# Kernel optimization log

Hardware: AMD Instinct MI355X
Metric: run time of the kernel (lower is better)

## Reference

```python
import jax, jax.numpy as jnp
import numpy as np

B, T, E, A, D, S, N, K = 256, 64, 1024, 32, 1024, 256, 1024, 5
MIN_STD = 0.1


def setup_inputs() -> dict:
    key = jax.random.key(0)
    ks = jax.random.split(key, 16)
    def w(k, shape, scale=0.02):
        return jax.random.normal(k, shape, jnp.float32) * scale
    return dict(
        seq_len=T,
        obs_embed=jax.random.normal(ks[0], (B, T, E), jnp.float32),
        action=jax.random.normal(ks[1], (B, T, A), jnp.float32),
        nonterms=jnp.ones((B, T, 1), jnp.float32),
        init_deter=jax.random.normal(ks[2], (B, D), jnp.float32),
        init_stoch=jax.random.normal(ks[3], (B, S), jnp.float32),
        noise_prior=jax.random.normal(ks[4], (T - 1, B, S), jnp.float32),
        noise_post=jax.random.normal(ks[5], (T - 1, B, S), jnp.float32),
        W_embed=w(ks[6], (S + A, D)), b_embed=jnp.zeros((D,), jnp.float32),
        W_ens=w(ks[7], (K, D, S)), b_ens=jnp.zeros((K, S), jnp.float32),
        W_ih=w(ks[8], (3 * D, D)), W_hh=w(ks[9], (3 * D, D)),
        b_ih=jnp.zeros((3 * D,), jnp.float32), b_hh=jnp.zeros((3 * D,), jnp.float32),
        Wp1=w(ks[10], (D, N)), bp1=jnp.zeros((N,), jnp.float32),
        Wp2=w(ks[11], (N, 2 * S)), bp2=jnp.zeros((2 * S,), jnp.float32),
        Wq1=w(ks[12], (D + E, N)), bq1=jnp.zeros((N,), jnp.float32),
        Wq2=w(ks[13], (N, 2 * S)), bq2=jnp.zeros((2 * S,), jnp.float32),
    )


def _rollout(obs_embed, action, nonterms, init_deter, init_stoch,
             noise_prior, noise_post, W_embed, b_embed, W_ens, b_ens,
             W_ih, W_hh, b_ih, b_hh, Wp1, bp1, Wp2, bp2, Wq1, bq1, Wq2, bq2):
    elu = jax.nn.elu

    def gru(x, h):  # torch.nn.GRUCell math
        gi = x @ W_ih.T + b_ih
        gh = h @ W_hh.T + b_hh
        ir, iz, ig = jnp.split(gi, 3, axis=-1)
        hr, hz, hg = jnp.split(gh, 3, axis=-1)
        r = jax.nn.sigmoid(ir + hr)
        z = jax.nn.sigmoid(iz + hz)
        n = jnp.tanh(ig + r * hg)
        return (1.0 - z) * n + z * h

    def step(carry, xs):
        deter, stoch = carry
        obs_t, act_t, nt, eps_p, eps_q = xs  # nt: [B,1]
        prev_action = act_t * nt
        sa = elu(jnp.concatenate([stoch * nt, prev_action], -1) @ W_embed + b_embed)
        preds = jnp.einsum('bd,kds->kbs', sa, W_ens) + b_ens[:, None, :]  # ensemble heads
        deter_new = gru(sa, deter * nt)
        pm, ps = jnp.split(elu(deter_new @ Wp1 + bp1) @ Wp2 + bp2, 2, -1)
        ps = jax.nn.softplus(ps) + MIN_STD
        prior_stoch = pm + ps * eps_p
        qm, qs = jnp.split(elu(jnp.concatenate([deter_new, obs_t], -1) @ Wq1 + bq1) @ Wq2 + bq2, 2, -1)
        qs = jax.nn.softplus(qs) + MIN_STD
        post_stoch = qm + qs * eps_q
        prior_cat = jnp.concatenate([pm, ps, prior_stoch, deter_new], -1)   # [B, 3S+D]
        post_cat = jnp.concatenate([qm, qs, post_stoch, deter_new], -1)     # [B, 3S+D]
        disag_flat = jnp.transpose(preds, (1, 0, 2)).reshape(preds.shape[1], -1)  # [B, K*S]
        out = jnp.concatenate([prior_cat, post_cat, disag_flat], -1)
        return (deter_new, post_stoch), out

    Tm1 = noise_prior.shape[0]
    xs = (jnp.swapaxes(obs_embed[:, :Tm1], 0, 1),
          jnp.swapaxes(action[:, :Tm1], 0, 1),
          jnp.swapaxes(nonterms[:, :Tm1], 0, 1),
          noise_prior, noise_post)
    _, outs = jax.lax.scan(step, (init_deter, init_stoch), xs)
    return jnp.swapaxes(outs, 0, 1)  # [B, T-1, 2*(3S+D)+K*S]


def reference(seq_len, obs_embed, action, nonterms, init_deter, init_stoch,
              noise_prior, noise_post, W_embed, b_embed, W_ens, b_ens,
              W_ih, W_hh, b_ih, b_hh, Wp1, bp1, Wp2, bp2, Wq1, bq1, Wq2, bq2):
    return _rollout(obs_embed, action, nonterms, init_deter, init_stoch,
                    noise_prior, noise_post, W_embed, b_embed, W_ens, b_ens,
                    W_ih, W_hh, b_ih, b_hh, Wp1, bp1, Wp2, bp2, Wq1, bq1, Wq2, bq2)
```

## Files before the change

kernel.cpp:

```cpp
#include <hip/hip_runtime.h>

typedef float f32x4 __attribute__((ext_vector_type(4)));
typedef __bf16 bf16x8 __attribute__((ext_vector_type(8)));
typedef unsigned short u16;

#define OUTC 4864
#define OUTT ((size_t)63 * OUTC)

__device__ __forceinline__ u16 f2bf(float f) {
    unsigned u = __float_as_uint(f);
    u += 0x7FFFu + ((u >> 16) & 1u);
    return (u16)(u >> 16);
}
__device__ __forceinline__ float bf2f(u16 h) { return __uint_as_float((unsigned)h << 16); }
__device__ __forceinline__ float fexp(float x) { return __expf(x); }
__device__ __forceinline__ float eluf(float x) { return x > 0.f ? x : fexp(x) - 1.f; }
__device__ __forceinline__ float splus(float x) { return x > 15.f ? x : __logf(1.f + fexp(x)); }
__device__ __forceinline__ float sigm(float x) { return 1.f / (1.f + fexp(-x)); }
__device__ __forceinline__ float tanhfast(float x) { return 2.f / (1.f + fexp(-2.f * x)) - 1.f; }
__device__ __forceinline__ int swz(int row, int cb) { return row * 128 + (cb ^ ((row & 7) << 4)); }

template <int NT, class FA, class FE>
__device__ __forceinline__ void gemmN(char* As, FA fa, const u16* __restrict__ Bt,
                                      int ldb, int n0, int nstr, int K, int m0, FE fe) {
    char* Bs = As + 8192;
    const int tid = threadIdx.x;
    const int lane = tid & 63;
    const int w = tid >> 6;
    const int wr = (w >> 1) * 32, wc = (w & 1) * 32;
    f32x4 acc[NT][4];
    f32x4 zf = {0.f, 0.f, 0.f, 0.f};
#pragma unroll
    for (int j = 0; j < NT; j++)
#pragma unroll
        for (int q = 0; q < 4; q++) acc[j][q] = zf;
    const int r0 = tid >> 3;
    const int ke = (tid & 7) * 8;
    const int cb = (tid & 7) * 16;
    uint4 av0 = fa(m0 + r0, ke);
    uint4 av1 = fa(m0 + r0 + 32, ke);
    uint4 bv[NT][2];
#pragma unroll
    for (int j = 0; j < NT; j++) {
        bv[j][0] = *(const uint4*)(Bt + (size_t)(n0 + j * nstr + r0) * ldb + ke);
        bv[j][1] = *(const uint4*)(Bt + (size_t)(n0 + j * nstr + r0 + 32) * ldb + ke);
    }
    for (int k0 = 0; k0 < K; k0 += 64) {
        __syncthreads();
        *(uint4*)(As + swz(r0, cb)) = av0;
        *(uint4*)(As + swz(r0 + 32, cb)) = av1;
#pragma unroll
        for (int j = 0; j < NT; j++) {
            char* B = Bs + j * 8192;
            *(uint4*)(B + swz(r0, cb)) = bv[j][0];
            *(uint4*)(B + swz(r0 + 32, cb)) = bv[j][1];
        }
        __syncthreads();
        if (k0 + 64 < K) {
            int k1 = k0 + 64 + ke;
            av0 = fa(m0 + r0, k1);
            av1 = fa(m0 + r0 + 32, k1);
#pragma unroll
            for (int j = 0; j < NT; j++) {
                bv[j][0] = *(const uint4*)(Bt + (size_t)(n0 + j * nstr + r0) * ldb + k1);
                bv[j][1] = *(const uint4*)(Bt + (size_t)(n0 + j * nstr + r0 + 32) * ldb + k1);
            }
        }
#pragma unroll
        for (int kk = 0; kk < 64; kk += 32) {
            const int fcb = kk * 2 + (lane >> 4) * 16;
            bf16x8 a0 = *(const bf16x8*)(As + swz(wr + (lane & 15), fcb));
            bf16x8 a1 = *(const bf16x8*)(As + swz(wr + 16 + (lane & 15), fcb));
#pragma unroll
            for (int j = 0; j < NT; j++) {
                char* B = Bs + j * 8192;
                bf16x8 b0 = *(const bf16x8*)(B + swz(wc + (lane & 15), fcb));
                bf16x8 b1 = *(const bf16x8*)(B + swz(wc + 16 + (lane & 15), fcb));
                acc[j][0] = __builtin_amdgcn_mfma_f32_16x16x32_bf16(a0, b0, acc[j][0], 0, 0, 0);
                acc[j][1] = __builtin_amdgcn_mfma_f32_16x16x32_bf16(a0, b1, acc[j][1], 0, 0, 0);
                acc[j][2] = __builtin_amdgcn_mfma_f32_16x16x32_bf16(a1, b0, acc[j][2], 0, 0, 0);
                acc[j][3] = __builtin_amdgcn_mfma_f32_16x16x32_bf16(a1, b1, acc[j][3], 0, 0, 0);
            }
        }
    }
    const int er = (lane >> 4) * 4, ec = lane & 15;
#pragma unroll
    for (int q = 0; q < 4; q++) {
        int rr = m0 + wr + (q >> 1) * 16 + er;
        int cc = n0 + wc + (q & 1) * 16 + ec;
#pragma unroll
        for (int r = 0; r < 4; r++) {
            float vals[NT];
#pragma unroll
            for (int j = 0; j < NT; j++) vals[j] = acc[j][q][r];
            fe(rr + r, cc, vals);
        }
    }
}

__global__ void __launch_bounds__(256) k_cast(const float* __restrict__ in,
                                              u16* __restrict__ out, int n) {
    int i = blockIdx.x * 256 + threadIdx.x;
    if (i < n) out[i] = f2bf(in[i]);
}

__global__ void __launch_bounds__(256) k_transpose(const float* __restrict__ in,
                                                   u16* __restrict__ out,
                                                   int R, int C, int Rpad, int total) {
    int i = blockIdx.x * 256 + threadIdx.x;
    if (i >= total) return;
    int r = i % Rpad;
    int bc = i / Rpad;
    int c = bc % C;
    int bb = bc / C;
    out[i] = (r < R) ? f2bf(in[((size_t)bb * R + r) * C + c]) : (u16)0;
}

__global__ void __launch_bounds__(256) k_init(const float* __restrict__ init_deter,
                                              const float* __restrict__ init_stoch,
                                              const float* __restrict__ action,
                                              const float* __restrict__ nonterms,
                                              float* __restrict__ deter,
                                              u16* __restrict__ h_nt,
                                              u16* __restrict__ x_embed) {
    int idx = blockIdx.x * 256 + threadIdx.x;
    int b = idx >> 10, d = idx & 1023;
    float nt0 = nonterms[b * 64];
    float dv = init_deter[idx];
    deter[idx] = dv;
    h_nt[idx] = f2bf(dv * nt0);
    if (d < 256) {
        x_embed[b * 320 + d] = f2bf(init_stoch[b * 256 + d] * nt0);
    } else if (d < 320) {
        int c = d - 256;
        x_embed[b * 320 + d] = (c < 32) ? f2bf(action[(size_t)b * 2048 + c] * nt0) : (u16)0;
    }
}

__global__ void __launch_bounds__(256) k_obsc(const float* __restrict__ obs,
                                              const u16* __restrict__ Wq1o_t,
                                              u16* __restrict__ OBSC) {
    __shared__ char sm[40960];
    int jid = blockIdx.x;
    int rb = jid >> 2, cg = jid & 3;
    int m0 = rb * 64, n0 = cg * 256;
    auto fa = [&](int r, int k) {
        int tt = r >> 8, bb = r & 255;
        const float* p = obs + ((size_t)bb * 64 + tt) * 1024 + k;
        float4 f0 = *(const float4*)p, f1 = *(const float4*)(p + 4);
        union { u16 h[8]; uint4 q; } x;
        x.h[0] = f2bf(f0.x); x.h[1] = f2bf(f0.y); x.h[2] = f2bf(f0.z); x.h[3] = f2bf(f0.w);
        x.h[4] = f2bf(f1.x); x.h[5] = f2bf(f1.y); x.h[6] = f2bf(f1.z); x.h[7] = f2bf(f1.w);
        return x.q;
    };
    auto fe = [&](int r, int n, const float* v) {
#pragma unroll
        for (int j = 0; j < 4; j++) OBSC[(size_t)r * 1024 + n + j * 64] = f2bf(v[j]);
    };
    gemmN<4>(sm, fa, Wq1o_t, 1024, n0, 64, 1024, m0, fe);
}

__global__ void __launch_bounds__(256) k_sa(const u16* __restrict__ xe,
                                            const u16* __restrict__ Wt,
                                            const float* __restrict__ bias,
                                            u16* __restrict__ sa) {
    __shared__ char sm[16384];
    int m0 = blockIdx.y * 64, n0 = blockIdx.x * 64;
    auto fa = [&](int r, int k) { return *(const uint4*)(xe + r * 320 + k); };
    auto fe = [&](int r, int n, const float* v) {
        sa[r * 1024 + n] = f2bf(eluf(v[0] + bias[n]));
    };
    gemmN<1>(sm, fa, Wt, 320, n0, 0, 320, m0, fe);
}

__global__ void __launch_bounds__(256) k_gemm3072(const u16* __restrict__ A,
                                                  const u16* __restrict__ B,
                                                  const float* __restrict__ bias,
                                                  float* __restrict__ dst) {
    __shared__ char sm[16384];
    int m0 = blockIdx.y * 64, n0 = blockIdx.x * 64;
    auto fa = [&](int r, int k) { return *(const uint4*)(A + r * 1024 + k); };
    auto fe = [&](int r, int n, const float* v) { dst[(size_t)r * 3072 + n] = v[0] + bias[n]; };
    gemmN<1>(sm, fa, B, 1024, n0, 0, 1024, m0, fe);
}

__global__ void __launch_bounds__(256) k_gru(const float* __restrict__ gi,
                                             const float* __restrict__ gh,
                                             float* __restrict__ deter,
                                             const float* __restrict__ nonterms, int t,
                                             u16* __restrict__ deter_hist,
                                             u16* __restrict__ h_nt,
                                             float* __restrict__ out) {
    int idx = blockIdx.x * 256 + threadIdx.x;
    int b = idx >> 10, d = idx & 1023;
    float nt = nonterms[b * 64 + t];
    float h = deter[idx] * nt;
    size_t gb = (size_t)b * 3072;
    float r = sigm(gi[gb + d] + gh[gb + d]);
    float z = sigm(gi[gb + 1024 + d] + gh[gb + 1024 + d]);
    float n = tanhfast(gi[gb + 2048 + d] + r * gh[gb + 2048 + d]);
    float dn = (1.f - z) * n + z * h;
    deter[idx] = dn;
    u16 db = f2bf(dn);
    deter_hist[(size_t)t * 262144 + idx] = db;
    h_nt[idx] = f2bf(dn * nonterms[b * 64 + t + 1]);
    float* ob = out + (size_t)b * OUTT + (size_t)t * OUTC;
    ob[768 + d] = dn;
    ob[2560 + d] = dn;
}

__global__ void __launch_bounds__(256) k_step4(const u16* __restrict__ h_nt,
                                               const u16* __restrict__ Whh_b,
                                               const float* __restrict__ b_hh,
                                               float* __restrict__ gh,
                                               const u16* __restrict__ deter_hist,
                                               const u16* __restrict__ Wq1d_t,
                                               const float* __restrict__ bq1,
                                               const u16* __restrict__ OBSC,
                                               u16* __restrict__ HQ, int t) {
    __shared__ char sm[16384];
    int bid = blockIdx.x;
    if (bid < 192) {
        if (t >= 62) return;
        int m0 = (bid / 48) * 64, n0 = (bid % 48) * 64;
        auto fa = [&](int r, int k) { return *(const uint4*)(h_nt + r * 1024 + k); };
        auto fe = [&](int r, int n, const float* v) { gh[(size_t)r * 3072 + n] = v[0] + b_hh[n]; };
        gemmN<1>(sm, fa, Whh_b, 1024, n0, 0, 1024, m0, fe);
    } else {
        int j = bid - 192;
        int m0 = (j / 16) * 64, n0 = (j % 16) * 64;
        const u16* A = deter_hist + (size_t)t * 262144;
        const u16* ob = OBSC + (size_t)t * 262144;
        auto fa = [&](int r, int k) { return *(const uint4*)(A + r * 1024 + k); };
        auto fe = [&](int r, int n, const float* v) {
            HQ[r * 1024 + n] = f2bf(eluf(v[0] + bq1[n] + bf2f(ob[r * 1024 + n])));
        };
        gemmN<1>(sm, fa, Wq1d_t, 1024, n0, 0, 1024, m0, fe);
    }
}

__global__ void __launch_bounds__(256) k_q2dist(const u16* __restrict__ HQ,
                                                const u16* __restrict__ Wq2_t,
                                                const float* __restrict__ bq2,
                                                const float* __restrict__ noise_q,
                                                const float* __restrict__ nonterms,
                                                const float* __restrict__ action,
                                                float* __restrict__ out,
                                                u16* __restrict__ x_embed, int t) {
    __shared__ char sm[24576];
    int bid = blockIdx.x;
    if (bid < 16) {
        int m0 = (bid >> 2) * 64, n0 = (bid & 3) * 64;
        auto fa = [&](int r, int k) { return *(const uint4*)(HQ + r * 1024 + k); };
        auto fe = [&](int r, int s, const float* v) {
            float m = v[0] + bq2[s];
            float sd = splus(v[1] + bq2[s + 256]) + 0.1f;
            float eps = noise_q[(size_t)t * 65536 + r * 256 + s];
            float st = m + sd * eps;
            float* obp = out + (size_t)r * OUTT + (size_t)t * OUTC + 1792;
            obp[s] = m;
            obp[256 + s] = sd;
            obp[512 + s] = st;
            float ntn = nonterms[r * 64 + t + 1];
            x_embed[r * 320 + s] = f2bf(st * ntn);
        };
        gemmN<2>(sm, fa, Wq2_t, 1024, n0, 256, 1024, m0, fe);
    } else {
        for (int i = (bid - 16) * 256 + threadIdx.x; i < 16384; i += 1024) {
            int b = i >> 6, c = i & 63;
            float ntn = nonterms[b * 64 + t + 1];
            u16 v = 0;
            if (c < 32) v = f2bf(action[(size_t)b * 2048 + (size_t)(t + 1) * 32 + c] * ntn);
            x_embed[b * 320 + 256 + c] = v;
        }
    }
}

__global__ void __launch_bounds__(256) k_ens(const u16* __restrict__ sa_hist,
                                             const u16* __restrict__ Wens_t,
                                             const float* __restrict__ b_ens,
                                             float* __restrict__ out) {
    __shared__ char sm[40960];
    int m0 = blockIdx.y * 64, n0 = blockIdx.x * 256;
    auto fa = [&](int r, int k) { return *(const uint4*)(sa_hist + (size_t)r * 1024 + k); };
    auto fe = [&](int r, int cc, const float* v) {
        int tt = r >> 8, b = r & 255;
        float* op = out + (size_t)b * OUTT + (size_t)tt * OUTC + 3584;
#pragma unroll
        for (int j = 0; j < 4; j++) {
            int n = cc + j * 64;
            op[n] = v[j] + b_ens[n];
        }
    };
    gemmN<4>(sm, fa, Wens_t, 1024, n0, 64, 1024, m0, fe);
}

__global__ void __launch_bounds__(256) k_hp(const u16* __restrict__ deter_hist,
                                            const u16* __restrict__ Wp1_t,
                                            const float* __restrict__ bp1,
                                            u16* __restrict__ HP) {
    __shared__ char sm[40960];
    int m0 = blockIdx.y * 64, n0 = blockIdx.x * 256;
    auto fa = [&](int r, int k) { return *(const uint4*)(deter_hist + (size_t)r * 1024 + k); };
    auto fe = [&](int r, int cc, const float* v) {
#pragma unroll
        for (int j = 0; j < 4; j++) {
            int n = cc + j * 64;
            HP[(size_t)r * 1024 + n] = f2bf(eluf(v[j] + bp1[n]));
        }
    };
    gemmN<4>(sm, fa, Wp1_t, 1024, n0, 64, 1024, m0, fe);
}

__global__ void __launch_bounds__(256) k_p2(const u16* __restrict__ HP,
                                            const u16* __restrict__ Wp2_t,
                                            const float* __restrict__ bp2,
                                            const float* __restrict__ noise_p,
                                            float* __restrict__ out) {
    __shared__ char sm[24576];
    int m0 = blockIdx.y * 64, n0 = blockIdx.x * 64;
    auto fa = [&](int r, int k) { return *(const uint4*)(HP + (size_t)r * 1024 + k); };
    auto fe = [&](int r, int s, const float* v) {
        int tt = r >> 8, b = r & 255;
        float m = v[0] + bp2[s];
        float sd = splus(v[1] + bp2[s + 256]) + 0.1f;
        float eps = noise_p[(size_t)tt * 65536 + b * 256 + s];
        float st = m + sd * eps;
        float* obp = out + (size_t)b * OUTT + (size_t)tt * OUTC;
        obp[s] = m;
        obp[256 + s] = sd;
        obp[512 + s] = st;
    };
    gemmN<2>(sm, fa, Wp2_t, 1024, n0, 256, 1024, m0, fe);
}

extern "C" void kernel_launch(void* const* d_in, const int* in_sizes, int n_in,
                              void* d_out, int out_size, void* d_ws, size_t ws_size,
                              hipStream_t stream) {
    const float* obs = (const float*)d_in[1];
    const float* action = (const float*)d_in[2];
    const float* nonterms = (const float*)d_in[3];
    const float* init_deter = (const float*)d_in[4];
    const float* init_stoch = (const float*)d_in[5];
    const float* noise_p = (const float*)d_in[6];
    const float* noise_q = (const float*)d_in[7];
    const float* W_embed = (const float*)d_in[8];
    const float* b_embed = (const float*)d_in[9];
    const float* W_ens = (const float*)d_in[10];
    const float* b_ens = (const float*)d_in[11];
    const float* W_ih = (const float*)d_in[12];
    const float* W_hh = (const float*)d_in[13];
    const float* b_ih = (const float*)d_in[14];
    const float* b_hh = (const float*)d_in[15];
    const float* Wp1 = (const float*)d_in[16];
    const float* bp1 = (const float*)d_in[17];
    const float* Wp2 = (const float*)d_in[18];
    const float* bp2 = (const float*)d_in[19];
    const float* Wq1 = (const float*)d_in[20];
    const float* bq1 = (const float*)d_in[21];
    const float* Wq2 = (const float*)d_in[22];
    const float* bq2 = (const float*)d_in[23];
    float* out = (float*)d_out;

    char* ws = (char*)d_ws;
    size_t off = 0;
    auto alloc = [&](size_t bytes) {
        void* p = ws + off;
        off += (bytes + 255) & ~(size_t)255;
        return p;
    };
    u16* Wembed_t = (u16*)alloc((size_t)1024 * 320 * 2);
    u16* Wih_b = (u16*)alloc((size_t)3072 * 1024 * 2);
    u16* Whh_b = (u16*)alloc((size_t)3072 * 1024 * 2);
    u16* Wens_t = (u16*)alloc((size_t)1280 * 1024 * 2);
    u16* Wp1_t = (u16*)alloc((size_t)1024 * 1024 * 2);
    u16* Wp2_t = (u16*)alloc((size_t)512 * 1024 * 2);
    u16* Wq1d_t = (u16*)alloc((size_t)1024 * 1024 * 2);
    u16* Wq1o_t = (u16*)alloc((size_t)1024 * 1024 * 2);
    u16* Wq2_t = (u16*)alloc((size_t)512 * 1024 * 2);
    u16* OBSC = (u16*)alloc((size_t)16128 * 1024 * 2);
    u16* sa_hist = (u16*)alloc((size_t)16128 * 1024 * 2);
    u16* deter_hist = (u16*)alloc((size_t)16128 * 1024 * 2);
    u16* x_embed = (u16*)alloc((size_t)256 * 320 * 2);
    u16* h_nt = (u16*)alloc((size_t)256 * 1024 * 2);
    u16* HQ = (u16*)alloc((size_t)256 * 1024 * 2);
    float* deter = (float*)alloc((size_t)256 * 1024 * 4);
    float* gi = (float*)alloc((size_t)256 * 3072 * 4);
    float* gh = (float*)alloc((size_t)256 * 3072 * 4);
    (void)ws_size; (void)in_sizes; (void)n_in; (void)out_size;

    {
        int tot = 1024 * 320;
        k_transpose<<<(tot + 255) / 256, 256, 0, stream>>>(W_embed, Wembed_t, 288, 1024, 320, tot);
        int nc = 3072 * 1024;
        k_cast<<<(nc + 255) / 256, 256, 0, stream>>>(W_ih, Wih_b, nc);
        k_cast<<<(nc + 255) / 256, 256, 0, stream>>>(W_hh, Whh_b, nc);
        tot = 5 * 256 * 1024;
        k_transpose<<<(tot + 255) / 256, 256, 0, stream>>>(W_ens, Wens_t, 1024, 256, 1024, tot);
        tot = 1024 * 1024;
        k_transpose<<<(tot + 255) / 256, 256, 0, stream>>>(Wp1, Wp1_t, 1024, 1024, 1024, tot);
        tot = 512 * 1024;
        k_transpose<<<(tot + 255) / 256, 256, 0, stream>>>(Wp2, Wp2_t, 1024, 512, 1024, tot);
        tot = 1024 * 1024;
        k_transpose<<<(tot + 255) / 256, 256, 0, stream>>>(Wq1, Wq1d_t, 1024, 1024, 1024, tot);
        k_transpose<<<(tot + 255) / 256, 256, 0, stream>>>(Wq1 + 1024 * 1024, Wq1o_t, 1024, 1024, 1024, tot);
        tot = 512 * 1024;
        k_transpose<<<(tot + 255) / 256, 256, 0, stream>>>(Wq2, Wq2_t, 1024, 512, 1024, tot);
    }
    k_init<<<1024, 256, 0, stream>>>(init_deter, init_stoch, action, nonterms,
                                     deter, h_nt, x_embed);
    k_obsc<<<1008, 256, 0, stream>>>(obs, Wq1o_t, OBSC);
    k_gemm3072<<<dim3(48, 4), 256, 0, stream>>>(h_nt, Whh_b, b_hh, gh);

    for (int t = 0; t < 63; t++) {
        u16* sa_t = sa_hist + (size_t)t * 262144;
        k_sa<<<dim3(16, 4), 256, 0, stream>>>(x_embed, Wembed_t, b_embed, sa_t);
        k_gemm3072<<<dim3(48, 4), 256, 0, stream>>>(sa_t, Wih_b, b_ih, gi);
        k_gru<<<1024, 256, 0, stream>>>(gi, gh, deter, nonterms, t, deter_hist, h_nt, out);
        k_step4<<<256, 256, 0, stream>>>(h_nt, Whh_b, b_hh, gh, deter_hist, Wq1d_t,
                                         bq1, OBSC, HQ, t);
        k_q2dist<<<20, 256, 0, stream>>>(HQ, Wq2_t, bq2, noise_q, nonterms, action,
                                         out, x_embed, t);
    }

    k_ens<<<dim3(5, 252), 256, 0, stream>>>(sa_hist, Wens_t, b_ens, out);
    u16* HP = OBSC;
    k_hp<<<dim3(4, 252), 256, 0, stream>>>(deter_hist, Wp1_t, bp1, HP);
    k_p2<<<dim3(4, 252), 256, 0, stream>>>(HP, Wp2_t, bp2, noise_p, out);
}
```

Before: 5.471 ms.

## Fuse GRU gate GEMM with cell update, merge prep kernels, double-buffer GEMM loads

Fuses the W_ih GEMM with the GRU elementwise update so the three gate columns are computed per block with NT=3, which removes the gi buffer and one launch per timestep. Merges all weight cast and transpose kernels plus init into one grid-stride prep kernel, and merges the initial gh GEMM into the obs-projection launch. The GEMM core gains a two-deep register prefetch (ping/pong) that hides global load latency. The trade-off is higher register pressure and a fused GRU kernel that launches only 64 blocks.

```diff
diff --git a/kernel.cpp b/kernel.cpp
--- a/kernel.cpp
+++ b/kernel.cpp
@@ -37,33 +37,62 @@
     const int r0 = tid >> 3;
     const int ke = (tid & 7) * 8;
     const int cb = (tid & 7) * 16;
-    uint4 av0 = fa(m0 + r0, ke);
-    uint4 av1 = fa(m0 + r0 + 32, ke);
-    uint4 bv[NT][2];
+    uint4 avP0, avP1, bvP[NT][2], avQ0, avQ1, bvQ[NT][2];
+    avP0 = fa(m0 + r0, ke);
+    avP1 = fa(m0 + r0 + 32, ke);
 #pragma unroll
     for (int j = 0; j < NT; j++) {
-        bv[j][0] = *(const uint4*)(Bt + (size_t)(n0 + j * nstr + r0) * ldb + ke);
-        bv[j][1] = *(const uint4*)(Bt + (size_t)(n0 + j * nstr + r0 + 32) * ldb + ke);
-    }
+        bvP[j][0] = *(const uint4*)(Bt + (size_t)(n0 + j * nstr + r0) * ldb + ke);
+        bvP[j][1] = *(const uint4*)(Bt + (size_t)(n0 + j * nstr + r0 + 32) * ldb + ke);
+    }
+    avQ0 = fa(m0 + r0, 64 + ke);
+    avQ1 = fa(m0 + r0 + 32, 64 + ke);
+#pragma unroll
+    for (int j = 0; j < NT; j++) {
+        bvQ[j][0] = *(const uint4*)(Bt + (size_t)(n0 + j * nstr + r0) * ldb + 64 + ke);
+        bvQ[j][1] = *(const uint4*)(Bt + (size_t)(n0 + j * nstr + r0 + 32) * ldb + 64 + ke);
+    }
+    bool ping = true;
     for (int k0 = 0; k0 < K; k0 += 64) {
         __syncthreads();
-        *(uint4*)(As + swz(r0, cb)) = av0;
-        *(uint4*)(As + swz(r0 + 32, cb)) = av1;
-#pragma unroll
-        for (int j = 0; j < NT; j++) {
-            char* B = Bs + j * 8192;
-            *(uint4*)(B + swz(r0, cb)) = bv[j][0];
-            *(uint4*)(B + swz(r0 + 32, cb)) = bv[j][1];
+        if (ping) {
+            *(uint4*)(As + swz(r0, cb)) = avP0;
+            *(uint4*)(As + swz(r0 + 32, cb)) = avP1;
+#pragma unroll
+            for (int j = 0; j < NT; j++) {
+                char* B = Bs + j * 8192;
+                *(uint4*)(B + swz(r0, cb)) = bvP[j][0];
+                *(uint4*)(B + swz(r0 + 32, cb)) = bvP[j][1];
+            }
+        } else {
+            *(uint4*)(As + swz(r0, cb)) = avQ0;
+            *(uint4*)(As + swz(r0 + 32, cb)) = avQ1;
+#pragma unroll
+            for (int j = 0; j < NT; j++) {
+                char* B = Bs + j * 8192;
+                *(uint4*)(B + swz(r0, cb)) = bvQ[j][0];
+                *(uint4*)(B + swz(r0 + 32, cb)) = bvQ[j][1];
+            }
         }
         __syncthreads();
-        if (k0 + 64 < K) {
-            int k1 = k0 + 64 + ke;
-            av0 = fa(m0 + r0, k1);
-            av1 = fa(m0 + r0 + 32, k1);
-#pragma unroll
-            for (int j = 0; j < NT; j++) {
-                bv[j][0] = *(const uint4*)(Bt + (size_t)(n0 + j * nstr + r0) * ldb + k1);
-                bv[j][1] = *(const uint4*)(Bt + (size_t)(n0 + j * nstr + r0 + 32) * ldb + k1);
+        if (k0 + 128 < K) {
+            int k1 = k0 + 128 + ke;
+            if (ping) {
+                avP0 = fa(m0 + r0, k1);
+                avP1 = fa(m0 + r0 + 32, k1);
+#pragma unroll
+                for (int j = 0; j < NT; j++) {
+                    bvP[j][0] = *(const uint4*)(Bt + (size_t)(n0 + j * nstr + r0) * ldb + k1);
+                    bvP[j][1] = *(const uint4*)(Bt + (size_t)(n0 + j * nstr + r0 + 32) * ldb + k1);
+                }
+            } else {
+                avQ0 = fa(m0 + r0, k1);
+                avQ1 = fa(m0 + r0 + 32, k1);
+#pragma unroll
+                for (int j = 0; j < NT; j++) {
+                    bvQ[j][0] = *(const uint4*)(Bt + (size_t)(n0 + j * nstr + r0) * ldb + k1);
+                    bvQ[j][1] = *(const uint4*)(Bt + (size_t)(n0 + j * nstr + r0 + 32) * ldb + k1);
+                }
             }
         }
 #pragma unroll
@@ -82,6 +111,7 @@
                 acc[j][3] = __builtin_amdgcn_mfma_f32_16x16x32_bf16(a1, b1, acc[j][3], 0, 0, 0);
             }
         }
+        ping = !ping;
     }
     const int er = (lane >> 4) * 4, ec = lane & 15;
 #pragma unroll
@@ -98,66 +128,88 @@
     }
 }
 
-__global__ void __launch_bounds__(256) k_cast(const float* __restrict__ in,
-                                              u16* __restrict__ out, int n) {
-    int i = blockIdx.x * 256 + threadIdx.x;
-    if (i < n) out[i] = f2bf(in[i]);
-}
-
-__global__ void __launch_bounds__(256) k_transpose(const float* __restrict__ in,
-                                                   u16* __restrict__ out,
-                                                   int R, int C, int Rpad, int total) {
-    int i = blockIdx.x * 256 + threadIdx.x;
-    if (i >= total) return;
-    int r = i % Rpad;
-    int bc = i / Rpad;
-    int c = bc % C;
-    int bb = bc / C;
-    out[i] = (r < R) ? f2bf(in[((size_t)bb * R + r) * C + c]) : (u16)0;
-}
-
-__global__ void __launch_bounds__(256) k_init(const float* __restrict__ init_deter,
-                                              const float* __restrict__ init_stoch,
-                                              const float* __restrict__ action,
-                                              const float* __restrict__ nonterms,
-                                              float* __restrict__ deter,
-                                              u16* __restrict__ h_nt,
-                                              u16* __restrict__ x_embed) {
-    int idx = blockIdx.x * 256 + threadIdx.x;
-    int b = idx >> 10, d = idx & 1023;
-    float nt0 = nonterms[b * 64];
-    float dv = init_deter[idx];
-    deter[idx] = dv;
-    h_nt[idx] = f2bf(dv * nt0);
-    if (d < 256) {
-        x_embed[b * 320 + d] = f2bf(init_stoch[b * 256 + d] * nt0);
-    } else if (d < 320) {
-        int c = d - 256;
-        x_embed[b * 320 + d] = (c < 32) ? f2bf(action[(size_t)b * 2048 + c] * nt0) : (u16)0;
-    }
-}
-
-__global__ void __launch_bounds__(256) k_obsc(const float* __restrict__ obs,
-                                              const u16* __restrict__ Wq1o_t,
-                                              u16* __restrict__ OBSC) {
+#define PREP_BLOCKS 2048
+#define PGSTR (PREP_BLOCKS * 256)
+__device__ __forceinline__ void tpose(const float* __restrict__ in, u16* __restrict__ out,
+                                      int R, int C, int Rpad, int total, int gtid) {
+    for (int i = gtid; i < total; i += PGSTR) {
+        int r = i % Rpad;
+        int bc = i / Rpad;
+        int c = bc % C;
+        int bb = bc / C;
+        out[i] = (r < R) ? f2bf(in[((size_t)bb * R + r) * C + c]) : (u16)0;
+    }
+}
+__device__ __forceinline__ void castb(const float* __restrict__ in, u16* __restrict__ out,
+                                      int total, int gtid) {
+    for (int i = gtid; i < total; i += PGSTR) out[i] = f2bf(in[i]);
+}
+
+__global__ void __launch_bounds__(256) k_prep(
+    const float* W_embed, const float* W_ih, const float* W_hh, const float* W_ens,
+    const float* Wp1, const float* Wp2, const float* Wq1, const float* Wq2,
+    u16* Wembed_t, u16* Wih_b, u16* Whh_b, u16* Wens_t,
+    u16* Wp1_t, u16* Wp2_t, u16* Wq1d_t, u16* Wq1o_t, u16* Wq2_t,
+    const float* init_deter, const float* init_stoch, const float* action,
+    const float* nonterms, float* deter, u16* h_nt, u16* x_embed) {
+    int gtid = blockIdx.x * 256 + threadIdx.x;
+    tpose(W_embed, Wembed_t, 288, 1024, 320, 1024 * 320, gtid);
+    castb(W_ih, Wih_b, 3072 * 1024, gtid);
+    castb(W_hh, Whh_b, 3072 * 1024, gtid);
+    tpose(W_ens, Wens_t, 1024, 256, 1024, 5 * 256 * 1024, gtid);
+    tpose(Wp1, Wp1_t, 1024, 1024, 1024, 1024 * 1024, gtid);
+    tpose(Wp2, Wp2_t, 1024, 512, 1024, 512 * 1024, gtid);
+    tpose(Wq1, Wq1d_t, 1024, 1024, 1024, 1024 * 1024, gtid);
+    tpose(Wq1 + 1024 * 1024, Wq1o_t, 1024, 1024, 1024, 1024 * 1024, gtid);
+    tpose(Wq2, Wq2_t, 1024, 512, 1024, 512 * 1024, gtid);
+    for (int idx = gtid; idx < 262144; idx += PGSTR) {
+        int b = idx >> 10, d = idx & 1023;
+        float nt0 = nonterms[b * 64];
+        float dv = init_deter[idx];
+        deter[idx] = dv;
+        h_nt[idx] = f2bf(dv * nt0);
+        if (d < 256) {
+            x_embed[b * 320 + d] = f2bf(init_stoch[b * 256 + d] * nt0);
+        } else if (d < 320) {
+            int c = d - 256;
+            x_embed[b * 320 + d] = (c < 32) ? f2bf(action[(size_t)b * 2048 + c] * nt0) : (u16)0;
+        }
+    }
+}
+
+__global__ void __launch_bounds__(256) k_obsc_gh0(const float* __restrict__ obs,
+                                                  const u16* __restrict__ Wq1o_t,
+                                                  u16* __restrict__ OBSC,
+                                                  const u16* __restrict__ h_nt,
+                                                  const u16* __restrict__ Whh_b,
+                                                  const float* __restrict__ b_hh,
+                                                  float* __restrict__ gh) {
     __shared__ char sm[40960];
-    int jid = blockIdx.x;
-    int rb = jid >> 2, cg = jid & 3;
-    int m0 = rb * 64, n0 = cg * 256;
-    auto fa = [&](int r, int k) {
-        int tt = r >> 8, bb = r & 255;
-        const float* p = obs + ((size_t)bb * 64 + tt) * 1024 + k;
-        float4 f0 = *(const float4*)p, f1 = *(const float4*)(p + 4);
-        union { u16 h[8]; uint4 q; } x;
-        x.h[0] = f2bf(f0.x); x.h[1] = f2bf(f0.y); x.h[2] = f2bf(f0.z); x.h[3] = f2bf(f0.w);
-        x.h[4] = f2bf(f1.x); x.h[5] = f2bf(f1.y); x.h[6] = f2bf(f1.z); x.h[7] = f2bf(f1.w);
-        return x.q;
-    };
-    auto fe = [&](int r, int n, const float* v) {
-#pragma unroll
-        for (int j = 0; j < 4; j++) OBSC[(size_t)r * 1024 + n + j * 64] = f2bf(v[j]);
-    };
-    gemmN<4>(sm, fa, Wq1o_t, 1024, n0, 64, 1024, m0, fe);
+    int bid = blockIdx.x;
+    if (bid < 1008) {
+        int rb = bid >> 2, cg = bid & 3;
+        int m0 = rb * 64, n0 = cg * 256;
+        auto fa = [&](int r, int k) {
+            int tt = r >> 8, bb = r & 255;
+            const float* p = obs + ((size_t)bb * 64 + tt) * 1024 + k;
+            float4 f0 = *(const float4*)p, f1 = *(const float4*)(p + 4);
+            union { u16 h[8]; uint4 q; } x;
+            x.h[0] = f2bf(f0.x); x.h[1] = f2bf(f0.y); x.h[2] = f2bf(f0.z); x.h[3] = f2bf(f0.w);
+            x.h[4] = f2bf(f1.x); x.h[5] = f2bf(f1.y); x.h[6] = f2bf(f1.z); x.h[7] = f2bf(f1.w);
+            return x.q;
+        };
+        auto fe = [&](int r, int n, const float* v) {
+#pragma unroll
+            for (int j = 0; j < 4; j++) OBSC[(size_t)r * 1024 + n + j * 64] = f2bf(v[j]);
+        };
+        gemmN<4>(sm, fa, Wq1o_t, 1024, n0, 64, 1024, m0, fe);
+    } else {
+        int j = bid - 1008;
+        int m0 = (j / 48) * 64, n0 = (j % 48) * 64;
+        auto fa = [&](int r, int k) { return *(const uint4*)(h_nt + r * 1024 + k); };
+        auto fe = [&](int r, int n, const float* v) { gh[(size_t)r * 3072 + n] = v[0] + b_hh[n]; };
+        gemmN<1>(sm, fa, Whh_b, 1024, n0, 0, 1024, m0, fe);
+    }
 }
 
 __global__ void __launch_bounds__(256) k_sa(const u16* __restrict__ xe,
@@ -173,43 +225,36 @@
     gemmN<1>(sm, fa, Wt, 320, n0, 0, 320, m0, fe);
 }
 
-__global__ void __launch_bounds__(256) k_gemm3072(const u16* __restrict__ A,
-                                                  const u16* __restrict__ B,
-                                                  const float* __restrict__ bias,
-                                                  float* __restrict__ dst) {
-    __shared__ char sm[16384];
+__global__ void __launch_bounds__(256) k_gi_gru(const u16* __restrict__ sa,
+                                                const u16* __restrict__ Wih_b,
+                                                const float* __restrict__ b_ih,
+                                                const float* __restrict__ gh,
+                                                const float* __restrict__ nonterms,
+                                                float* __restrict__ deter,
+                                                u16* __restrict__ deter_hist,
+                                                u16* __restrict__ h_nt,
+                                                float* __restrict__ out, int t) {
+    __shared__ char sm[32768];
     int m0 = blockIdx.y * 64, n0 = blockIdx.x * 64;
-    auto fa = [&](int r, int k) { return *(const uint4*)(A + r * 1024 + k); };
-    auto fe = [&](int r, int n, const float* v) { dst[(size_t)r * 3072 + n] = v[0] + bias[n]; };
-    gemmN<1>(sm, fa, B, 1024, n0, 0, 1024, m0, fe);
-}
-
-__global__ void __launch_bounds__(256) k_gru(const float* __restrict__ gi,
-                                             const float* __restrict__ gh,
-                                             float* __restrict__ deter,
-                                             const float* __restrict__ nonterms, int t,
-                                             u16* __restrict__ deter_hist,
-                                             u16* __restrict__ h_nt,
-                                             float* __restrict__ out) {
-    int idx = blockIdx.x * 256 + threadIdx.x;
-    int b = idx >> 10, d = idx & 1023;
-    float nt = nonterms[b * 64 + t];
-    float h = deter[idx] * nt;
-    size_t gb = (size_t)b * 3072;
-    float r = sigm(gi[gb + d] + gh[gb + d]);
-    float z = sigm(gi[gb + 1024 + d] + gh[gb + 1024 + d]);
-    float n = tanhfast(gi[gb + 2048 + d] + r * gh[gb + 2048 + d]);
-    float dn = (1.f - z) * n + z * h;
-    deter[idx] = dn;
-    u16 db = f2bf(dn);
-    deter_hist[(size_t)t * 262144 + idx] = db;
-    h_nt[idx] = f2bf(dn * nonterms[b * 64 + t + 1]);
-    float* ob = out + (size_t)b * OUTT + (size_t)t * OUTC;
-    ob[768 + d] = dn;
-    ob[2560 + d] = dn;
-}
-
-__global__ void __launch_bounds__(256) k_step4(const u16* __restrict__ h_nt,
+    auto fa = [&](int r, int k) { return *(const uint4*)(sa + r * 1024 + k); };
+    auto fe = [&](int r, int d, const float* v) {
+        size_t gb = (size_t)r * 3072;
+        float rg = sigm(v[0] + b_ih[d] + gh[gb + d]);
+        float zg = sigm(v[1] + b_ih[1024 + d] + gh[gb + 1024 + d]);
+        float ng = tanhfast(v[2] + b_ih[2048 + d] + rg * gh[gb + 2048 + d]);
+        float h = deter[r * 1024 + d] * nonterms[r * 64 + t];
+        float dn = (1.f - zg) * ng + zg * h;
+        deter[r * 1024 + d] = dn;
+        deter_hist[(size_t)t * 262144 + r * 1024 + d] = f2bf(dn);
+        h_nt[r * 1024 + d] = f2bf(dn * nonterms[r * 64 + t + 1]);
+        float* ob = out + (size_t)r * OUTT + (size_t)t * OUTC;
+        ob[768 + d] = dn;
+        ob[2560 + d] = dn;
+    };
+    gemmN<3>(sm, fa, Wih_b, 1024, n0, 1024, 1024, m0, fe);
+}
+
+__global__ void __launch_bounds__(256) k_step3(const u16* __restrict__ h_nt,
                                                const u16* __restrict__ Whh_b,
                                                const float* __restrict__ b_hh,
                                                float* __restrict__ gh,
@@ -385,39 +430,21 @@
     u16* h_nt = (u16*)alloc((size_t)256 * 1024 * 2);
     u16* HQ = (u16*)alloc((size_t)256 * 1024 * 2);
     float* deter = (float*)alloc((size_t)256 * 1024 * 4);
-    float* gi = (float*)alloc((size_t)256 * 3072 * 4);
     float* gh = (float*)alloc((size_t)256 * 3072 * 4);
     (void)ws_size; (void)in_sizes; (void)n_in; (void)out_size;
 
-    {
-        int tot = 1024 * 320;
-        k_transpose<<<(tot + 255) / 256, 256, 0, stream>>>(W_embed, Wembed_t, 288, 1024, 320, tot);
-        int nc = 3072 * 1024;
-        k_cast<<<(nc + 255) / 256, 256, 0, stream>>>(W_ih, Wih_b, nc);
-        k_cast<<<(nc + 255) / 256, 256, 0, stream>>>(W_hh, Whh_b, nc);
-        tot = 5 * 256 * 1024;
-        k_transpose<<<(tot + 255) / 256, 256, 0, stream>>>(W_ens, Wens_t, 1024, 256, 1024, tot);
-        tot = 1024 * 1024;
-        k_transpose<<<(tot + 255) / 256, 256, 0, stream>>>(Wp1, Wp1_t, 1024, 1024, 1024, tot);
-        tot = 512 * 1024;
-        k_transpose<<<(tot + 255) / 256, 256, 0, stream>>>(Wp2, Wp2_t, 1024, 512, 1024, tot);
-        tot = 1024 * 1024;
-        k_transpose<<<(tot + 255) / 256, 256, 0, stream>>>(Wq1, Wq1d_t, 1024, 1024, 1024, tot);
-        k_transpose<<<(tot + 255) / 256, 256, 0, stream>>>(Wq1 + 1024 * 1024, Wq1o_t, 1024, 1024, 1024, tot);
-        tot = 512 * 1024;
-        k_transpose<<<(tot + 255) / 256, 256, 0, stream>>>(Wq2, Wq2_t, 1024, 512, 1024, tot);
-    }
-    k_init<<<1024, 256, 0, stream>>>(init_deter, init_stoch, action, nonterms,
-                                     deter, h_nt, x_embed);
-    k_obsc<<<1008, 256, 0, stream>>>(obs, Wq1o_t, OBSC);
-    k_gemm3072<<<dim3(48, 4), 256, 0, stream>>>(h_nt, Whh_b, b_hh, gh);
+    k_prep<<<PREP_BLOCKS, 256, 0, stream>>>(
+        W_embed, W_ih, W_hh, W_ens, Wp1, Wp2, Wq1, Wq2,
+        Wembed_t, Wih_b, Whh_b, Wens_t, Wp1_t, Wp2_t, Wq1d_t, Wq1o_t, Wq2_t,
+        init_deter, init_stoch, action, nonterms, deter, h_nt, x_embed);
+    k_obsc_gh0<<<1200, 256, 0, stream>>>(obs, Wq1o_t, OBSC, h_nt, Whh_b, b_hh, gh);
 
     for (int t = 0; t < 63; t++) {
         u16* sa_t = sa_hist + (size_t)t * 262144;
         k_sa<<<dim3(16, 4), 256, 0, stream>>>(x_embed, Wembed_t, b_embed, sa_t);
-        k_gemm3072<<<dim3(48, 4), 256, 0, stream>>>(sa_t, Wih_b, b_ih, gi);
-        k_gru<<<1024, 256, 0, stream>>>(gi, gh, deter, nonterms, t, deter_hist, h_nt, out);
-        k_step4<<<256, 256, 0, stream>>>(h_nt, Whh_b, b_hh, gh, deter_hist, Wq1d_t,
+        k_gi_gru<<<dim3(16, 4), 256, 0, stream>>>(sa_t, Wih_b, b_ih, gh, nonterms,
+                                                  deter, deter_hist, h_nt, out, t);
+        k_step3<<<256, 256, 0, stream>>>(h_nt, Whh_b, b_hh, gh, deter_hist, Wq1d_t,
                                          bq1, OBSC, HQ, t);
         k_q2dist<<<20, 256, 0, stream>>>(HQ, Wq2_t, bq2, noise_q, nonterms, action,
                                          out, x_embed, t);
```

Measured after the change: 6.739 ms. 1.23x slower.
